# Kernel optimization log

Hardware: AMD Instinct MI355X
Metric: run time of the kernel (lower is better)

Reference implementation:

```python
import jax, jax.numpy as jnp
import numpy as np

NUP, NDOWN = 15, 15
NELEC = NUP + NDOWN
NATOMS = 10
NDIM = 3
NBATCH = 512
FEAT = 64   # hidden feature dim
K_RBF = 64  # gaussian RBF expansion size
NLAYERS = 2
RBF_CUT = 8.0


def _build_graphs():
    # elec-elec: upper-tri pairs, each pair -> 2 directed edges (i->j, j->i),
    # matching ree.repeat_interleave(2) edge-distance ordering.
    ii, jj = np.triu_indices(NELEC, k=1)                      # [435]
    ee_src = np.stack([ii, jj], 1).reshape(-1).astype(np.int32)  # [870]
    ee_dst = np.stack([jj, ii], 1).reshape(-1).astype(np.int32)
    ee_types = np.array([0] * NUP + [1] * NDOWN, np.int32)
    # elec-nuc: nodes = [electrons(0..29), atoms(30..39)];
    # ren is transposed to [natoms, nelec] then flattened -> atom-major pair order.
    aa = np.repeat(np.arange(NATOMS), NELEC)
    ee_ = np.tile(np.arange(NELEC), NATOMS)
    en_src = np.stack([ee_, NELEC + aa], 1).reshape(-1).astype(np.int32)  # [600]
    en_dst = np.stack([NELEC + aa, ee_], 1).reshape(-1).astype(np.int32)
    en_types = np.concatenate([np.array([0] * NUP + [1] * NDOWN),
                               2 + np.arange(NATOMS)]).astype(np.int32)
    return ee_src, ee_dst, ee_types, en_src, en_dst, en_types


def setup_inputs() -> dict:
    key = jax.random.key(0)
    ks = jax.random.split(key, 20)
    ee_src, ee_dst, ee_types, en_src, en_dst, en_types = _build_graphs()
    s = 0.1
    inp = {
        "pos": jax.random.normal(ks[0], (NBATCH, NELEC * NDIM), jnp.float32) * 2.0,
        "atoms": jax.random.normal(ks[1], (NATOMS, NDIM), jnp.float32) * 3.0,
        "emb_ee": jax.random.normal(ks[2], (2, FEAT), jnp.float32) * s,
        "wf_ee": jax.random.normal(ks[3], (K_RBF, FEAT), jnp.float32) * s,
        "bf_ee": jnp.zeros((FEAT,), jnp.float32),
        "wl_ee": jax.random.normal(ks[4], (NLAYERS, FEAT, FEAT), jnp.float32) * s,
        "bl_ee": jnp.zeros((NLAYERS, FEAT), jnp.float32),
        "wr_ee": jax.random.normal(ks[5], (FEAT, 1), jnp.float32) * s,
        "br_ee": jnp.zeros((1,), jnp.float32),
        "emb_en": jax.random.normal(ks[6], (2 + NATOMS, FEAT), jnp.float32) * s,
        "wf_en": jax.random.normal(ks[7], (K_RBF, FEAT), jnp.float32) * s,
        "bf_en": jnp.zeros((FEAT,), jnp.float32),
        "wl_en": jax.random.normal(ks[8], (NLAYERS, FEAT, FEAT), jnp.float32) * s,
        "bl_en": jnp.zeros((NLAYERS, FEAT), jnp.float32),
        "wr_en": jax.random.normal(ks[9], (FEAT, 1), jnp.float32) * s,
        "br_en": jnp.zeros((1,), jnp.float32),
        "ee_src": jnp.asarray(ee_src), "ee_dst": jnp.asarray(ee_dst),
        "ee_types": jnp.asarray(ee_types),
        "en_src": jnp.asarray(en_src), "en_dst": jnp.asarray(en_dst),
        "en_types": jnp.asarray(en_types),
    }
    return inp


def _gnn_kernel(types, src, dst, edist, emb, wf, bf, wl, bl, wr, br):
    """MGCN-style interaction net on a batch of identical graphs.
    types [N] int, src/dst [E] int, edist [nb, E] float."""
    nb = edist.shape[0]
    N = types.shape[0]
    centers = jnp.linspace(0.0, RBF_CUT, K_RBF).astype(edist.dtype)
    rbf = jnp.exp(-(edist[..., None] - centers) ** 2)        # [nb, E, K]
    filt = jnp.tanh(rbf @ wf + bf)                           # [nb, E, F]
    h = jnp.broadcast_to(emb[types][None], (nb, N, emb.shape[1]))  # [nb, N, F]
    for l in range(wl.shape[0]):
        m = h[:, src, :] * filt                              # gather + edge filter
        agg = jnp.zeros_like(h).at[:, dst, :].add(m)         # scatter-add messages
        h = h + jnp.tanh(agg @ wl[l] + bl[l])
    return h.sum(axis=1) @ wr + br                           # [nb, 1] readout


def reference(pos, atoms, emb_ee, wf_ee, bf_ee, wl_ee, bl_ee, wr_ee, br_ee,
              emb_en, wf_en, bf_en, wl_en, bl_en, wr_en, br_en,
              ee_src, ee_dst, ee_types, en_src, en_dst, en_types):
    nb = pos.shape[0]
    xyz = pos.reshape(nb, NELEC, NDIM)
    # elec-elec edge distances (src/dst index electron nodes; symmetric so this
    # equals extract_tri_up(...).repeat_interleave(2))
    d_ee = jnp.linalg.norm(xyz[:, ee_src] - xyz[:, ee_dst], axis=-1)   # [nb, 870]
    # elec-nuc: node positions = [electrons; atoms]
    nodepos = jnp.concatenate(
        [xyz, jnp.broadcast_to(atoms[None], (nb, NATOMS, NDIM))], axis=1)
    d_en = jnp.linalg.norm(nodepos[:, en_src] - nodepos[:, en_dst], axis=-1)  # [nb, 600]
    ee_k = _gnn_kernel(ee_types, ee_src, ee_dst, d_ee,
                       emb_ee, wf_ee, bf_ee, wl_ee, bl_ee, wr_ee, br_ee)
    en_k = _gnn_kernel(en_types, en_src, en_dst, d_en,
                       emb_en, wf_en, bf_en, wl_en, bl_en, wr_en, br_en)
    return jnp.exp(ee_k + en_k)   # [nb, 1] Jastrow factor (derivative=0)
```

## Files before the change

### kernel.cpp

```cpp
#include <hip/hip_runtime.h>
#include <math.h>

#define NB      512
#define NELEC   30
#define NATOMS  10
#define NNEN    40
#define FEAT    64
#define KRBF    64
#define BLOCK   1024
#define NWAVES  (BLOCK/64)
#define NPEE    435
#define NPEN    300
#define TILE    32
#define FPAD    65
#define WROW    64

#define OFF_XYZ    0
#define OFF_AXYZ   96
#define OFF_KEE    128
#define H0_OFF     132
#define H1_OFF     (H0_OFF + NNEN*FEAT)
#define WR_OFF     (H1_OFF + NNEN*FEAT)
#define FILT_OFF   (WR_OFF + NWAVES*WROW)
#define SM_TOTAL   (FILT_OFF + NPEE*FPAD)

__device__ __forceinline__ int ee_base(int i) { return 29*i - ((i*(i-1))>>1); }

__device__ __forceinline__ void ee_layer(const float* __restrict__ hc,
                                         float* __restrict__ hn,
                                         const float* __restrict__ filt,
                                         float* __restrict__ wr,
                                         const float* __restrict__ wlL,
                                         const float* __restrict__ blL,
                                         int w, int lane)
{
    for (int i = w; i < NELEC; i += NWAVES) {
        float a = 0.f;
        #pragma unroll
        for (int j = 0; j < NELEC; ++j) {
            if (j != i) {
                int pp = (j < i) ? (ee_base(j) + (i - j - 1))
                                 : (ee_base(i) + (j - i - 1));
                a = fmaf(hc[j*FEAT + lane], filt[pp*FPAD + lane], a);
            }
        }
        wr[lane] = a;
        float a2 = 0.f;
        const float4* arow = reinterpret_cast<const float4*>(wr);
        #pragma unroll
        for (int k = 0; k < FEAT/4; ++k) {
            float4 av = arow[k];
            a2 = fmaf(av.x, wlL[(4*k+0)*FEAT + lane], a2);
            a2 = fmaf(av.y, wlL[(4*k+1)*FEAT + lane], a2);
            a2 = fmaf(av.z, wlL[(4*k+2)*FEAT + lane], a2);
            a2 = fmaf(av.w, wlL[(4*k+3)*FEAT + lane], a2);
        }
        hn[i*FEAT + lane] = hc[i*FEAT + lane] + tanhf(a2 + blL[lane]);
    }
}

__device__ __forceinline__ void en_layer(const float* __restrict__ hc,
                                         float* __restrict__ hn,
                                         const float* __restrict__ filt,
                                         float* __restrict__ wr,
                                         const float* __restrict__ wlL,
                                         const float* __restrict__ blL,
                                         int w, int lane)
{
    for (int n = w; n < NNEN; n += NWAVES) {
        float a = 0.f;
        if (n < NELEC) {
            #pragma unroll
            for (int at = 0; at < NATOMS; ++at)
                a = fmaf(hc[(NELEC+at)*FEAT + lane],
                         filt[(at*NELEC + n)*FPAD + lane], a);
        } else {
            const int at = n - NELEC;
            #pragma unroll
            for (int e2 = 0; e2 < NELEC; ++e2)
                a = fmaf(hc[e2*FEAT + lane],
                         filt[(at*NELEC + e2)*FPAD + lane], a);
        }
        wr[lane] = a;
        float a2 = 0.f;
        const float4* arow = reinterpret_cast<const float4*>(wr);
        #pragma unroll
        for (int k = 0; k < FEAT/4; ++k) {
            float4 av = arow[k];
            a2 = fmaf(av.x, wlL[(4*k+0)*FEAT + lane], a2);
            a2 = fmaf(av.y, wlL[(4*k+1)*FEAT + lane], a2);
            a2 = fmaf(av.z, wlL[(4*k+2)*FEAT + lane], a2);
            a2 = fmaf(av.w, wlL[(4*k+3)*FEAT + lane], a2);
        }
        hn[n*FEAT + lane] = hc[n*FEAT + lane] + tanhf(a2 + blL[lane]);
    }
}

__device__ __forceinline__ void rbf_filter(float dd, const float* __restrict__ wf,
                                           const float* __restrict__ bf,
                                           int uoff, float* __restrict__ dstrow)
{
    float facc[TILE];
    const float* bfH = bf + uoff;
    #pragma unroll
    for (int f = 0; f < TILE; ++f) facc[f] = bfH[f];
    #pragma unroll 2
    for (int k = 0; k < KRBF; ++k) {
        const float ck = (float)((double)k * (8.0/63.0));
        const float t  = dd - ck;
        const float rk = expf(-t*t);
        const float* wrow = wf + k*FEAT + uoff;
        #pragma unroll
        for (int f = 0; f < TILE; ++f) facc[f] = fmaf(rk, wrow[f], facc[f]);
    }
    #pragma unroll
    for (int ff = 0; ff < TILE; ++ff) dstrow[uoff + ff] = tanhf(facc[ff]);
}

__global__ __launch_bounds__(BLOCK)
void fused_kernel(const float* __restrict__ pos,
                  const float* __restrict__ atoms,
                  const float* __restrict__ emb_ee,
                  const float* __restrict__ wf_ee,
                  const float* __restrict__ bf_ee,
                  const float* __restrict__ wl_ee,
                  const float* __restrict__ bl_ee,
                  const float* __restrict__ wr_ee,
                  const float* __restrict__ br_ee,
                  const float* __restrict__ emb_en,
                  const float* __restrict__ wf_en,
                  const float* __restrict__ bf_en,
                  const float* __restrict__ wl_en,
                  const float* __restrict__ bl_en,
                  const float* __restrict__ wr_en,
                  const float* __restrict__ br_en,
                  const int*   __restrict__ ee_ty,
                  const int*   __restrict__ en_ty,
                  float*       __restrict__ out)
{
    extern __shared__ float sm[];
    float*  xyz  = sm + OFF_XYZ;
    float*  axyz = sm + OFF_AXYZ;
    double* keeP = reinterpret_cast<double*>(sm + OFF_KEE);
    float*  h0   = sm + H0_OFF;
    float*  h1   = sm + H1_OFF;
    float*  wrS  = sm + WR_OFF;
    float*  filt = sm + FILT_OFF;

    const int tid  = threadIdx.x;
    const int b    = blockIdx.x;
    const int lane = tid & 63;
    const int w    = tid >> 6;
    const int q    = tid & 511;
    const int uoff = __builtin_amdgcn_readfirstlane((tid >> 9) * TILE);
    float* wr = wrS + w*WROW;

    for (int idx = tid; idx < NELEC*3; idx += BLOCK) xyz[idx] = pos[b*NELEC*3 + idx];
    for (int idx = tid; idx < NATOMS*3; idx += BLOCK) axyz[idx] = atoms[idx];
    for (int idx = tid; idx < NELEC*FEAT; idx += BLOCK) {
        int n = idx >> 6, f = idx & 63;
        h0[idx] = emb_ee[ee_ty[n]*FEAT + f];
    }
    __syncthreads();

    if (q < NPEE) {
        const int p = q;
        int i = 0, rem = p;
        while (rem >= NELEC - 1 - i) { rem -= NELEC - 1 - i; ++i; }
        const int j = i + 1 + rem;
        const float dx = xyz[3*i+0] - xyz[3*j+0];
        const float dy = xyz[3*i+1] - xyz[3*j+1];
        const float dz = xyz[3*i+2] - xyz[3*j+2];
        const float dd = sqrtf(dx*dx + dy*dy + dz*dz);
        rbf_filter(dd, wf_ee, bf_ee, uoff, filt + p*FPAD);
    }
    __syncthreads();

    ee_layer(h0, h1, filt, wr, wl_ee + 0*FEAT*FEAT, bl_ee + 0*FEAT, w, lane);
    __syncthreads();
    ee_layer(h1, h0, filt, wr, wl_ee + 1*FEAT*FEAT, bl_ee + 1*FEAT, w, lane);
    __syncthreads();

    for (int idx = tid; idx < NNEN*FEAT; idx += BLOCK) {
        int n = idx >> 6, f = idx & 63;
        h1[idx] = emb_en[en_ty[n]*FEAT + f];
    }
    {
        const int v = w & 7;
        const int blk = (w < 8) ? (v < 5 ? v : -1)
                                : ((v >= 1 && v <= 3) ? v - 1
                                   : (v == 5 || v == 6) ? v - 2 : -1);
        if (blk >= 0) {
            const int p = blk*64 + lane;
            if (p < NPEN) {
                const int a = p / NELEC;
                const int e = p - a*NELEC;
                const float dx = xyz[3*e+0] - axyz[3*a+0];
                const float dy = xyz[3*e+1] - axyz[3*a+1];
                const float dz = xyz[3*e+2] - axyz[3*a+2];
                const float dd = sqrtf(dx*dx + dy*dy + dz*dz);
                rbf_filter(dd, wf_en, bf_en, uoff, filt + p*FPAD);
            }
        }
    }
    if (w == 0) {
        float s = 0.f;
        #pragma unroll
        for (int n = 0; n < NELEC; ++n) s += h0[n*FEAT + lane];
        double dv = (double)s * (double)wr_ee[lane];
        #pragma unroll
        for (int o = 32; o > 0; o >>= 1) dv += __shfl_xor(dv, o, 64);
        if (lane == 0) *keeP = dv + (double)br_ee[0];
    }
    __syncthreads();

    en_layer(h1, h0, filt, wr, wl_en + 0*FEAT*FEAT, bl_en + 0*FEAT, w, lane);
    __syncthreads();
    en_layer(h0, h1, filt, wr, wl_en + 1*FEAT*FEAT, bl_en + 1*FEAT, w, lane);
    __syncthreads();

    if (w == 0) {
        float s = 0.f;
        #pragma unroll
        for (int n = 0; n < NNEN; ++n) s += h1[n*FEAT + lane];
        double dv = (double)s * (double)wr_en[lane];
        #pragma unroll
        for (int o = 32; o > 0; o >>= 1) dv += __shfl_xor(dv, o, 64);
        if (lane == 0) out[b] = (float)exp(dv + (double)br_en[0] + *keeP);
    }
}

extern "C" void kernel_launch(void* const* d_in, const int* in_sizes, int n_in,
                              void* d_out, int out_size, void* d_ws, size_t ws_size,
                              hipStream_t stream) {
    const float* pos    = (const float*)d_in[0];
    const float* atoms  = (const float*)d_in[1];
    const float* emb_ee = (const float*)d_in[2];
    const float* wf_ee  = (const float*)d_in[3];
    const float* bf_ee  = (const float*)d_in[4];
    const float* wl_ee  = (const float*)d_in[5];
    const float* bl_ee  = (const float*)d_in[6];
    const float* wr_ee  = (const float*)d_in[7];
    const float* br_ee  = (const float*)d_in[8];
    const float* emb_en = (const float*)d_in[9];
    const float* wf_en  = (const float*)d_in[10];
    const float* bf_en  = (const float*)d_in[11];
    const float* wl_en  = (const float*)d_in[12];
    const float* bl_en  = (const float*)d_in[13];
    const float* wr_en  = (const float*)d_in[14];
    const float* br_en  = (const float*)d_in[15];
    const int*   ee_ty  = (const int*)d_in[18];
    const int*   en_ty  = (const int*)d_in[21];

    float* out = (float*)d_out;

    (void)hipFuncSetAttribute((const void*)fused_kernel,
            hipFuncAttributeMaxDynamicSharedMemorySize, SM_TOTAL*(int)sizeof(float));

    fused_kernel<<<NB, BLOCK, SM_TOTAL*sizeof(float), stream>>>(
        pos, atoms,
        emb_ee, wf_ee, bf_ee, wl_ee, bl_ee, wr_ee, br_ee,
        emb_en, wf_en, bf_en, wl_en, bl_en, wr_en, br_en,
        ee_ty, en_ty, out);
}
```

Baseline: 215.8 us.

## Stage RBF filter weights in LDS and rebalance wave work assignment

The RBF weight matrices wf and bf are copied into shared memory before each filter stage, so the per-thread inner loop reads LDS instead of global memory. The ee filter work is remapped so waves 0-6 and 7-13 take the two feature halves, and the en embedding fill is given to otherwise idle waves. Loop indices in the layer loops are made wave-uniform with readfirstlane. The cost is an extra block-wide copy and a barrier before the en filter stage, plus more LDS per block, which could lower occupancy.

```diff
diff --git a/kernel.cpp b/kernel.cpp
--- a/kernel.cpp
+++ b/kernel.cpp
@@ -13,18 +13,41 @@
 #define NPEN    300
 #define TILE    32
 #define FPAD    65
-#define WROW    64
-
-#define OFF_XYZ    0
-#define OFF_AXYZ   96
-#define OFF_KEE    128
-#define H0_OFF     132
-#define H1_OFF     (H0_OFF + NNEN*FEAT)
-#define WR_OFF     (H1_OFF + NNEN*FEAT)
-#define FILT_OFF   (WR_OFF + NWAVES*WROW)
-#define SM_TOTAL   (FILT_OFF + NPEE*FPAD)
+
+#define OFF_XYZ   0
+#define OFF_AXYZ  96
+#define OFF_KEE   128
+#define H0_OFF    132
+#define H1_OFF    (H0_OFF + NNEN*FEAT)
+#define FILT_OFF  (H1_OFF + NNEN*FEAT)
+#define WR_OFF    33528
+#define WF_OFF    (WR_OFF + NWAVES*64)
+#define BF_OFF    (WF_OFF + KRBF*FEAT)
+#define SM_TOTAL  (BF_OFF + FEAT)
 
 __device__ __forceinline__ int ee_base(int i) { return 29*i - ((i*(i-1))>>1); }
+
+__device__ __forceinline__ void rbf_filter(float dd,
+                                           const float* __restrict__ wfS,
+                                           const float* __restrict__ bfS,
+                                           int uoff, float* __restrict__ dstrow)
+{
+    float facc[TILE];
+    const float* bfH = bfS + uoff;
+    #pragma unroll
+    for (int f = 0; f < TILE; ++f) facc[f] = bfH[f];
+    #pragma unroll 2
+    for (int k = 0; k < KRBF; ++k) {
+        const float ck = (float)((double)k * (8.0/63.0));
+        const float t  = dd - ck;
+        const float rk = expf(-t*t);
+        const float* wrow = wfS + k*FEAT + uoff;
+        #pragma unroll
+        for (int f = 0; f < TILE; ++f) facc[f] = fmaf(rk, wrow[f], facc[f]);
+    }
+    #pragma unroll
+    for (int ff = 0; ff < TILE; ++ff) dstrow[uoff + ff] = tanhf(facc[ff]);
+}
 
 __device__ __forceinline__ void ee_layer(const float* __restrict__ hc,
                                          float* __restrict__ hn,
@@ -35,12 +58,13 @@
                                          int w, int lane)
 {
     for (int i = w; i < NELEC; i += NWAVES) {
+        const int iu = __builtin_amdgcn_readfirstlane(i);
         float a = 0.f;
         #pragma unroll
         for (int j = 0; j < NELEC; ++j) {
-            if (j != i) {
-                int pp = (j < i) ? (ee_base(j) + (i - j - 1))
-                                 : (ee_base(i) + (j - i - 1));
+            if (j != iu) {
+                int pp = (j < iu) ? (ee_base(j) + (iu - j - 1))
+                                  : (ee_base(iu) + (j - iu - 1));
                 a = fmaf(hc[j*FEAT + lane], filt[pp*FPAD + lane], a);
             }
         }
@@ -55,7 +79,7 @@
             a2 = fmaf(av.z, wlL[(4*k+2)*FEAT + lane], a2);
             a2 = fmaf(av.w, wlL[(4*k+3)*FEAT + lane], a2);
         }
-        hn[i*FEAT + lane] = hc[i*FEAT + lane] + tanhf(a2 + blL[lane]);
+        hn[iu*FEAT + lane] = hc[iu*FEAT + lane] + tanhf(a2 + blL[lane]);
     }
 }
 
@@ -68,14 +92,15 @@
                                          int w, int lane)
 {
     for (int n = w; n < NNEN; n += NWAVES) {
+        const int nu = __builtin_amdgcn_readfirstlane(n);
         float a = 0.f;
-        if (n < NELEC) {
+        if (nu < NELEC) {
             #pragma unroll
             for (int at = 0; at < NATOMS; ++at)
                 a = fmaf(hc[(NELEC+at)*FEAT + lane],
-                         filt[(at*NELEC + n)*FPAD + lane], a);
+                         filt[(at*NELEC + nu)*FPAD + lane], a);
         } else {
-            const int at = n - NELEC;
+            const int at = nu - NELEC;
             #pragma unroll
             for (int e2 = 0; e2 < NELEC; ++e2)
                 a = fmaf(hc[e2*FEAT + lane],
@@ -92,29 +117,8 @@
             a2 = fmaf(av.z, wlL[(4*k+2)*FEAT + lane], a2);
             a2 = fmaf(av.w, wlL[(4*k+3)*FEAT + lane], a2);
         }
-        hn[n*FEAT + lane] = hc[n*FEAT + lane] + tanhf(a2 + blL[lane]);
-    }
-}
-
-__device__ __forceinline__ void rbf_filter(float dd, const float* __restrict__ wf,
-                                           const float* __restrict__ bf,
-                                           int uoff, float* __restrict__ dstrow)
-{
-    float facc[TILE];
-    const float* bfH = bf + uoff;
-    #pragma unroll
-    for (int f = 0; f < TILE; ++f) facc[f] = bfH[f];
-    #pragma unroll 2
-    for (int k = 0; k < KRBF; ++k) {
-        const float ck = (float)((double)k * (8.0/63.0));
-        const float t  = dd - ck;
-        const float rk = expf(-t*t);
-        const float* wrow = wf + k*FEAT + uoff;
-        #pragma unroll
-        for (int f = 0; f < TILE; ++f) facc[f] = fmaf(rk, wrow[f], facc[f]);
-    }
-    #pragma unroll
-    for (int ff = 0; ff < TILE; ++ff) dstrow[uoff + ff] = tanhf(facc[ff]);
+        hn[nu*FEAT + lane] = hc[nu*FEAT + lane] + tanhf(a2 + blL[lane]);
+    }
 }
 
 __global__ __launch_bounds__(BLOCK)
@@ -144,35 +148,57 @@
     double* keeP = reinterpret_cast<double*>(sm + OFF_KEE);
     float*  h0   = sm + H0_OFF;
     float*  h1   = sm + H1_OFF;
+    float*  filt = sm + FILT_OFF;
     float*  wrS  = sm + WR_OFF;
-    float*  filt = sm + FILT_OFF;
+    float*  wfS  = sm + WF_OFF;
+    float*  bfS  = sm + BF_OFF;
 
     const int tid  = threadIdx.x;
     const int b    = blockIdx.x;
     const int lane = tid & 63;
     const int w    = tid >> 6;
     const int q    = tid & 511;
-    const int uoff = __builtin_amdgcn_readfirstlane((tid >> 9) * TILE);
-    float* wr = wrS + w*WROW;
+    float* wr = wrS + w*64;
+
+    const int  ee_t   = (w >= 7) ? 1 : 0;
+    const int  ee_p   = ((w >= 7 ? w - 7 : w) << 6) | lane;
+    const bool ee_ok  = (w < 14) && (ee_p < NPEE);
+    const int  v      = w & 7;
+    const int  en_blk = (w < 8) ? (v < 5 ? v : -1)
+                                : ((v >= 1 && v <= 3) ? v - 1
+                                   : (v == 5 || v == 6) ? v - 2 : -1);
+    const int  en_t   = (w >= 8) ? 1 : 0;
+    const int  en_p   = (en_blk < 0) ? 0 : ((en_blk << 6) | lane);
+    const bool en_ok  = (en_blk >= 0) && (en_p < NPEN);
+    const int  hr     = (w == 5) ? 0 : (w == 6) ? 1 : (w == 7) ? 2
+                      : (w == 8) ? 3 : (w == 12) ? 4 : -1;
+
+    const int uoff_ee = __builtin_amdgcn_readfirstlane(ee_t * TILE);
+    const int uoff_en = __builtin_amdgcn_readfirstlane(en_t * TILE);
 
     for (int idx = tid; idx < NELEC*3; idx += BLOCK) xyz[idx] = pos[b*NELEC*3 + idx];
     for (int idx = tid; idx < NATOMS*3; idx += BLOCK) axyz[idx] = atoms[idx];
+    {
+        const float4* src = reinterpret_cast<const float4*>(wf_ee);
+        float4* dst = reinterpret_cast<float4*>(wfS);
+        dst[tid] = src[tid];
+        if (tid < FEAT) bfS[tid] = bf_ee[tid];
+    }
     for (int idx = tid; idx < NELEC*FEAT; idx += BLOCK) {
         int n = idx >> 6, f = idx & 63;
         h0[idx] = emb_ee[ee_ty[n]*FEAT + f];
     }
     __syncthreads();
 
-    if (q < NPEE) {
-        const int p = q;
-        int i = 0, rem = p;
+    if (ee_ok) {
+        int i = 0, rem = ee_p;
         while (rem >= NELEC - 1 - i) { rem -= NELEC - 1 - i; ++i; }
         const int j = i + 1 + rem;
         const float dx = xyz[3*i+0] - xyz[3*j+0];
         const float dy = xyz[3*i+1] - xyz[3*j+1];
         const float dz = xyz[3*i+2] - xyz[3*j+2];
         const float dd = sqrtf(dx*dx + dy*dy + dz*dz);
-        rbf_filter(dd, wf_ee, bf_ee, uoff, filt + p*FPAD);
+        rbf_filter(dd, wfS, bfS, uoff_ee, filt + ee_p*FPAD);
     }
     __syncthreads();
 
@@ -181,29 +207,13 @@
     ee_layer(h1, h0, filt, wr, wl_ee + 1*FEAT*FEAT, bl_ee + 1*FEAT, w, lane);
     __syncthreads();
 
-    for (int idx = tid; idx < NNEN*FEAT; idx += BLOCK) {
-        int n = idx >> 6, f = idx & 63;
-        h1[idx] = emb_en[en_ty[n]*FEAT + f];
-    }
     {
-        const int v = w & 7;
-        const int blk = (w < 8) ? (v < 5 ? v : -1)
-                                : ((v >= 1 && v <= 3) ? v - 1
-                                   : (v == 5 || v == 6) ? v - 2 : -1);
-        if (blk >= 0) {
-            const int p = blk*64 + lane;
-            if (p < NPEN) {
-                const int a = p / NELEC;
-                const int e = p - a*NELEC;
-                const float dx = xyz[3*e+0] - axyz[3*a+0];
-                const float dy = xyz[3*e+1] - axyz[3*a+1];
-                const float dz = xyz[3*e+2] - axyz[3*a+2];
-                const float dd = sqrtf(dx*dx + dy*dy + dz*dz);
-                rbf_filter(dd, wf_en, bf_en, uoff, filt + p*FPAD);
-            }
-        }
-    }
-    if (w == 0) {
+        const float4* src = reinterpret_cast<const float4*>(wf_en);
+        float4* dst = reinterpret_cast<float4*>(wfS);
+        dst[tid] = src[tid];
+        if (tid < FEAT) bfS[tid] = bf_en[tid];
+    }
+    if (w == 15) {
         float s = 0.f;
         #pragma unroll
         for (int n = 0; n < NELEC; ++n) s += h0[n*FEAT + lane];
@@ -211,6 +221,24 @@
         #pragma unroll
         for (int o = 32; o > 0; o >>= 1) dv += __shfl_xor(dv, o, 64);
         if (lane == 0) *keeP = dv + (double)br_ee[0];
+    }
+    __syncthreads();
+
+    if (en_ok) {
+        const int a = en_p / NELEC;
+        const int e = en_p - a*NELEC;
+        const float dx = xyz[3*e+0] - axyz[3*a+0];
+        const float dy = xyz[3*e+1] - axyz[3*a+1];
+        const float dz = xyz[3*e+2] - axyz[3*a+2];
+        const float dd = sqrtf(dx*dx + dy*dy + dz*dz);
+        rbf_filter(dd, wfS, bfS, uoff_en, filt + en_p*FPAD);
+    }
+    if (hr >= 0) {
+        #pragma unroll
+        for (int r = 0; r < 8; ++r) {
+            const int idx = hr*64 + lane + r*320;
+            h1[idx] = emb_en[en_ty[idx >> 6]*FEAT + (idx & 63)];
+        }
     }
     __syncthreads();
 
```

New measurement: 264.9 us. +22.8%, slower.
